# Performance work log

Hardware: AMD Instinct MI355X
Metric: run time of the kernel (lower is better)

## Reference

```python
import jax, jax.numpy as jnp
import numpy as np

B, N = 32, 64
ATTR, STATE, REL, GDIM = 4, 8, 4, 32
NF = 128

def _ln(x, w, b, eps=1e-5):
    mu = jnp.mean(x, axis=-1, keepdims=True)
    var = jnp.mean((x - mu) ** 2, axis=-1, keepdims=True)
    return (x - mu) * jax.lax.rsqrt(var + eps) * w + b

def setup_inputs() -> dict:
    key = jax.random.key(0)
    ks = iter(jax.random.split(key, 32))
    d = {}
    d['attrs'] = jax.random.normal(next(ks), (B, N, ATTR), jnp.float32)
    d['states'] = jax.random.normal(next(ks), (B, N, STATE), jnp.float32)
    d['actions'] = jnp.zeros((B, N, 4), jnp.float32)  # action=False, unused
    d['rel_attrs'] = jax.random.normal(next(ks), (B, N, N, REL), jnp.float32)
    def w(shape):
        return jax.random.normal(next(ks), shape, jnp.float32) * 0.05
    d['oe_w0'] = w((NF, ATTR + STATE)); d['oe_b0'] = jnp.zeros((NF,), jnp.float32)
    d['oe_w1'] = w((NF, NF));            d['oe_b1'] = jnp.zeros((NF,), jnp.float32)
    d['re_w0'] = w((NF, STATE + REL + 2 * ATTR)); d['re_b0'] = jnp.zeros((NF,), jnp.float32)
    d['re_w1'] = w((NF, NF));            d['re_b1'] = jnp.zeros((NF,), jnp.float32)
    d['rp_w'] = w((NF, NF + 2 * NF));    d['rp_b'] = jnp.zeros((NF,), jnp.float32)
    d['rp_lnw'] = jnp.ones((NF,), jnp.float32); d['rp_lnb'] = jnp.zeros((NF,), jnp.float32)
    d['pp_w'] = w((NF, 2 * NF));         d['pp_b'] = jnp.zeros((NF,), jnp.float32)
    d['pp_lnw'] = jnp.ones((NF,), jnp.float32); d['pp_lnb'] = jnp.zeros((NF,), jnp.float32)
    d['pr_w0'] = w((NF, NF));            d['pr_b0'] = jnp.zeros((NF,), jnp.float32)
    d['pr_w1'] = w((GDIM, NF));          d['pr_b1'] = jnp.zeros((GDIM,), jnp.float32)
    d['pstep'] = 2
    return d

def reference(attrs, states, actions, rel_attrs,
              oe_w0, oe_b0, oe_w1, oe_b1,
              re_w0, re_b0, re_w1, re_b1,
              rp_w, rp_b, rp_lnw, rp_lnb,
              pp_w, pp_b, pp_lnw, pp_lnb,
              pr_w0, pr_b0, pr_w1, pr_b1, pstep):
    lin = lambda x, w, b: jnp.einsum('...i,oi->...o', x, w) + b
    # ---- encode nodes: [B,N,attr+state] -> [B,N,NF] (action=False) ----
    obj_in = jnp.concatenate([attrs, states], axis=2)
    obj_encode = jax.nn.relu(lin(jax.nn.relu(lin(obj_in, oe_w0, oe_b0)), oe_w1, oe_b1))
    # ---- encode edges over dense N x N pairs ----
    rel_states = states[:, :, None, :] - states[:, None, :, :]        # B,N,N,state
    recv_attr = jnp.broadcast_to(attrs[:, :, None, :], (attrs.shape[0], attrs.shape[1], attrs.shape[1], attrs.shape[2]))
    send_attr = jnp.broadcast_to(attrs[:, None, :, :], recv_attr.shape)
    rel_in = jnp.concatenate([rel_attrs, rel_states, recv_attr, send_attr], axis=3)
    rel_encode = jax.nn.relu(lin(jax.nn.relu(lin(rel_in, re_w0, re_b0)), re_w1, re_b1))  # B,N,N,NF
    # ---- propagation steps ----
    for _ in range(pstep):
        sh = rel_encode.shape[:3] + (obj_encode.shape[-1],)
        recv = jnp.broadcast_to(obj_encode[:, :, None, :], sh)
        send = jnp.broadcast_to(obj_encode[:, None, :, :], sh)
        rel_effect = jax.nn.relu(_ln(lin(jnp.concatenate([rel_encode, recv, send], axis=3), rp_w, rp_b), rp_lnw, rp_lnb))
        rel_agg = rel_effect.sum(axis=2)                               # B,N,NF
        obj_encode = jax.nn.relu(_ln(lin(jnp.concatenate([obj_encode, rel_agg], axis=2), pp_w, pp_b), pp_lnw, pp_lnb))
    # ---- predict + tanh (state_encoder has tanh=True) ----
    out = lin(jax.nn.relu(lin(obj_encode, pr_w0, pr_b0)), pr_w1, pr_b1)
    return jnp.tanh(out)
```

## Files before the change

kernel.cpp:

```cpp
#include <hip/hip_runtime.h>
#include <hip/hip_bf16.h>


#define ROWS 2048
typedef unsigned short u16;
typedef unsigned int u32;
typedef __attribute__((ext_vector_type(8))) short bf16x8;
typedef __attribute__((ext_vector_type(4))) float f32x4;

__device__ __forceinline__ float bsu(u16 u) { return __uint_as_float(((u32)u) << 16); }
__device__ __forceinline__ u16 f2b(float f) {
    u32 u = __float_as_uint(f);
    u32 r = (u + 0x7fffu + ((u >> 16) & 1u)) >> 16;
    return (u16)r;
}
__device__ __forceinline__ u32 pk2(float a, float b) {
    __hip_bfloat162 h = __float22bfloat162_rn(float2{a, b});
    union { __hip_bfloat162 h; u32 u; } c; c.h = h; return c.u;
}
__device__ __forceinline__ bf16x8 ldcvt8(const float* __restrict__ p) {
    float4 a = *(const float4*)p;
    float4 b = *(const float4*)(p + 4);
    union { u32 u[4]; bf16x8 v; } x;
    x.u[0] = pk2(a.x, a.y); x.u[1] = pk2(a.z, a.w);
    x.u[2] = pk2(b.x, b.y); x.u[3] = pk2(b.z, b.w);
    return x.v;
}

__global__ __launch_bounds__(256)
void k_node(const float* __restrict__ attrs, const float* __restrict__ states,
            const float* __restrict__ oe_w0, const float* __restrict__ oe_b0,
            const float* __restrict__ oe_w1, const float* __restrict__ oe_b1,
            const float* __restrict__ re_w0, const float* __restrict__ re_b0,
            const float* __restrict__ rp_w,  const float* __restrict__ rp_b,
            const float* __restrict__ re_w1, const float* __restrict__ pp_w,
            const float* __restrict__ pr_w0, const float* __restrict__ pr_w1,
            u16* __restrict__ re_w1b, u16* __restrict__ web, u16* __restrict__ pp_wb,
            u16* __restrict__ wrecvb, u16* __restrict__ wsendb,
            u16* __restrict__ pr_w0b, u16* __restrict__ pr_w1b,
            u16* __restrict__ objb, float* __restrict__ nr, float* __restrict__ ns,
            float* __restrict__ recvT, float* __restrict__ sendT)
{
    const int r0 = blockIdx.x * 16;
    const int t = threadIdx.x;
    __shared__ float xs[16][12];
    __shared__ float w0s[1536];
    __shared__ float rw0s[2560];
    __shared__ __align__(16) u16 hb[16 * 136];
    __shared__ __align__(16) u16 ob[16 * 136];

    {
        int gid = blockIdx.x * 256 + t;
        for (int i = gid; i < 118784; i += 32768) {
            int idx = i;
            if (idx < 16384) { re_w1b[idx] = f2b(re_w1[idx]); continue; }
            idx -= 16384;
            if (idx < 16384) { web[idx] = f2b(rp_w[(idx >> 7) * 384 + (idx & 127)]); continue; }
            idx -= 16384;
            if (idx < 32768) { pp_wb[idx] = f2b(pp_w[idx]); continue; }
            idx -= 32768;
            if (idx < 16384) { wrecvb[idx] = f2b(rp_w[(idx >> 7) * 384 + 128 + (idx & 127)]); continue; }
            idx -= 16384;
            if (idx < 16384) { wsendb[idx] = f2b(rp_w[(idx >> 7) * 384 + 256 + (idx & 127)]); continue; }
            idx -= 16384;
            if (idx < 16384) { pr_w0b[idx] = f2b(pr_w0[idx]); continue; }
            idx -= 16384;
            pr_w1b[idx] = f2b(pr_w1[idx]);
        }
    }

    if (t < 192) { int row = t / 12, c = t - row * 12;
        xs[row][c] = (c < 4) ? attrs[(r0 + row) * 4 + c] : states[(r0 + row) * 8 + (c - 4)]; }
    for (int i = t; i < 1536; i += 256) w0s[i] = oe_w0[i];
    for (int i = t; i < 2560; i += 256) rw0s[i] = re_w0[i];
    __syncthreads();

    for (int e = t; e < 2048; e += 256) {
        int row = e >> 7, o = e & 127;
        float h = oe_b0[o];
#pragma unroll
        for (int k = 0; k < 12; k++) h += w0s[o * 12 + k] * xs[row][k];
        hb[row * 136 + o] = f2b(fmaxf(h, 0.f));
        float s0 = 0.f, a0 = 0.f, a1 = 0.f;
#pragma unroll
        for (int k = 0; k < 8; k++) s0 += rw0s[o * 20 + 4 + k] * xs[row][4 + k];
#pragma unroll
        for (int k = 0; k < 4; k++) {
            a0 += rw0s[o * 20 + 12 + k] * xs[row][k];
            a1 += rw0s[o * 20 + 16 + k] * xs[row][k];
        }
        nr[(r0 + row) * 128 + o] = s0 + a0 + re_b0[o];
        ns[(r0 + row) * 128 + o] = a1 - s0;
    }
    __syncthreads();

    const int wave = t >> 6, lane = t & 63, tx = lane & 15, quad = lane >> 4;

    bf16x8 afr[4];
#pragma unroll
    for (int kk = 0; kk < 4; kk++) afr[kk] = *(const bf16x8*)&hb[tx * 136 + kk * 32 + quad * 8];
    f32x4 acc[2]; acc[0] = (f32x4){0.f,0.f,0.f,0.f}; acc[1] = acc[0];
#pragma unroll
    for (int ot = 0; ot < 2; ot++) {
        int o = (wave * 2 + ot) * 16 + tx;
#pragma unroll
        for (int kk = 0; kk < 4; kk++) {
            bf16x8 bfr = ldcvt8(&oe_w1[o * 128 + kk * 32 + quad * 8]);
            acc[ot] = __builtin_amdgcn_mfma_f32_16x16x32_bf16(afr[kk], bfr, acc[ot], 0, 0, 0);
        }
    }
#pragma unroll
    for (int ot = 0; ot < 2; ot++) {
        int o = (wave * 2 + ot) * 16 + tx;
        float bia = oe_b1[o];
#pragma unroll
        for (int r = 0; r < 4; r++)
            ob[(quad * 4 + r) * 136 + o] = f2b(fmaxf(acc[ot][r] + bia, 0.f));
    }
    __syncthreads();
    { int m = t >> 4, c = t & 15;
      *(uint4*)&objb[(r0 + m) * 128 + c * 8] = *(const uint4*)&ob[m * 136 + c * 8]; }

#pragma unroll
    for (int kk = 0; kk < 4; kk++) afr[kk] = *(const bf16x8*)&ob[tx * 136 + kk * 32 + quad * 8];
    f32x4 ar[2], an[2];
    ar[0] = (f32x4){0.f,0.f,0.f,0.f}; ar[1] = ar[0]; an[0] = ar[0]; an[1] = ar[0];
#pragma unroll
    for (int ot = 0; ot < 2; ot++) {
        int o = (wave * 2 + ot) * 16 + tx;
#pragma unroll
        for (int kk = 0; kk < 4; kk++) {
            bf16x8 br = ldcvt8(&rp_w[o * 384 + 128 + kk * 32 + quad * 8]);
            ar[ot] = __builtin_amdgcn_mfma_f32_16x16x32_bf16(afr[kk], br, ar[ot], 0, 0, 0);
            bf16x8 bs = ldcvt8(&rp_w[o * 384 + 256 + kk * 32 + quad * 8]);
            an[ot] = __builtin_amdgcn_mfma_f32_16x16x32_bf16(afr[kk], bs, an[ot], 0, 0, 0);
        }
    }
#pragma unroll
    for (int ot = 0; ot < 2; ot++) {
        int o = (wave * 2 + ot) * 16 + tx;
        float rb = rp_b[o];
#pragma unroll
        for (int r = 0; r < 4; r++) {
            recvT[(r0 + quad * 4 + r) * 128 + o] = ar[ot][r] + rb;
            sendT[(r0 + quad * 4 + r) * 128 + o] = an[ot][r];
        }
    }
}

__global__ __launch_bounds__(256, 4)
void k_edge_fused(const float* __restrict__ rel_attrs,
                  const float* __restrict__ re_w0, const u16* __restrict__ re_w1b,
                  const u16* __restrict__ web, const float* __restrict__ re_b1,
                  const float* __restrict__ rp_lnw, const float* __restrict__ rp_lnb,
                  const float* __restrict__ nr, const float* __restrict__ ns,
                  const float* __restrict__ recvT, const float* __restrict__ sendT,
                  u16* __restrict__ Ebuf, u16* __restrict__ aggb)
{
    const int blkg = blockIdx.x;
    const int b = blkg >> 6;
    const int t = threadIdx.x;
    __shared__ __align__(16) u16 hsb[64 * 144];
    __shared__ float lnws[128], lnbs[128];
    __shared__ float redS[256], redQ[256];

    if (t < 128) { lnws[t] = rp_lnw[t]; lnbs[t] = rp_lnb[t]; }

    {
        const int o0 = (t & 15) * 8;
        const int jb = t >> 4;
        float4 nr0 = *(const float4*)&nr[blkg * 128 + o0];
        float4 nr1 = *(const float4*)&nr[blkg * 128 + o0 + 4];
        float4 wreg[8];
#pragma unroll
        for (int k = 0; k < 8; k++) wreg[k] = *(const float4*)&re_w0[(o0 + k) * 20];
#pragma unroll
        for (int it = 0; it < 4; it++) {
            int j = jb + it * 16;
            float4 ra = *(const float4*)&rel_attrs[((size_t)blkg * 64 + j) * 4];
            const float* nsp = &ns[(b * 64 + j) * 128 + o0];
            float4 na = *(const float4*)nsp;
            float4 nb = *(const float4*)(nsp + 4);
            float v[8];
            v[0] = nr0.x + na.x; v[1] = nr0.y + na.y; v[2] = nr0.z + na.z; v[3] = nr0.w + na.w;
            v[4] = nr1.x + nb.x; v[5] = nr1.y + nb.y; v[6] = nr1.z + nb.z; v[7] = nr1.w + nb.w;
#pragma unroll
            for (int k = 0; k < 8; k++) {
                v[k] += wreg[k].x * ra.x + wreg[k].y * ra.y + wreg[k].z * ra.z + wreg[k].w * ra.w;
                v[k] = fmaxf(v[k], 0.f);
            }
            union { u32 u[4]; uint4 q; } p;
            p.u[0] = pk2(v[0], v[1]); p.u[1] = pk2(v[2], v[3]);
            p.u[2] = pk2(v[4], v[5]); p.u[3] = pk2(v[6], v[7]);
            *(uint4*)&hsb[j * 144 + o0] = p.q;
        }
    }

    const int w = t >> 6, lane = t & 63, tx = lane & 15, quad = lane >> 4;
    const int ob = w * 32;

    bf16x8 b1[2][4];
#pragma unroll
    for (int ot = 0; ot < 2; ot++)
#pragma unroll
        for (int kk = 0; kk < 4; kk++)
            b1[ot][kk] = *(const bf16x8*)&re_w1b[(ob + ot * 16 + tx) * 128 + kk * 32 + quad * 8];
    __syncthreads();

    f32x4 acc[4][2];
#pragma unroll
    for (int jt = 0; jt < 4; jt++) { acc[jt][0] = (f32x4){0.f,0.f,0.f,0.f}; acc[jt][1] = acc[jt][0]; }
#pragma unroll
    for (int jt = 0; jt < 4; jt++) {
        bf16x8 afr[4];
#pragma unroll
        for (int kk = 0; kk < 4; kk++)
            afr[kk] = *(const bf16x8*)&hsb[(jt * 16 + tx) * 144 + kk * 32 + quad * 8];
#pragma unroll
        for (int ot = 0; ot < 2; ot++)
#pragma unroll
            for (int kk = 0; kk < 4; kk++)
                acc[jt][ot] = __builtin_amdgcn_mfma_f32_16x16x32_bf16(afr[kk], b1[ot][kk], acc[jt][ot], 0, 0, 0);
    }
    __syncthreads();

    {
        float bia0 = re_b1[ob + tx], bia1 = re_b1[ob + 16 + tx];
#pragma unroll
        for (int jt = 0; jt < 4; jt++)
#pragma unroll
            for (int r = 0; r < 4; r++) {
                int j = jt * 16 + quad * 4 + r;
                hsb[j * 144 + ob + tx]      = f2b(fmaxf(acc[jt][0][r] + bia0, 0.f));
                hsb[j * 144 + ob + 16 + tx] = f2b(fmaxf(acc[jt][1][r] + bia1, 0.f));
            }
    }
    bf16x8 b2[2][4];
#pragma unroll
    for (int ot = 0; ot < 2; ot++)
#pragma unroll
        for (int kk = 0; kk < 4; kk++)
            b2[ot][kk] = *(const bf16x8*)&web[(ob + ot * 16 + tx) * 128 + kk * 32 + quad * 8];
    __syncthreads();

    f32x4 acc2[4][2];
#pragma unroll
    for (int jt = 0; jt < 4; jt++) { acc2[jt][0] = (f32x4){0.f,0.f,0.f,0.f}; acc2[jt][1] = acc2[jt][0]; }
#pragma unroll
    for (int jt = 0; jt < 4; jt++) {
        bf16x8 afr[4];
#pragma unroll
        for (int kk = 0; kk < 4; kk++)
            afr[kk] = *(const bf16x8*)&hsb[(jt * 16 + tx) * 144 + kk * 32 + quad * 8];
#pragma unroll
        for (int ot = 0; ot < 2; ot++)
#pragma unroll
            for (int kk = 0; kk < 4; kk++)
                acc2[jt][ot] = __builtin_amdgcn_mfma_f32_16x16x32_bf16(afr[kk], b2[ot][kk], acc2[jt][ot], 0, 0, 0);
    }

#pragma unroll
    for (int jt = 0; jt < 4; jt++)
#pragma unroll
        for (int ot = 0; ot < 2; ot++) {
            uint2 ev;
            ev.x = pk2(acc2[jt][ot][0], acc2[jt][ot][1]);
            ev.y = pk2(acc2[jt][ot][2], acc2[jt][ot][3]);
            *(uint2*)(Ebuf + ((size_t)((blkg * 4 + jt) * 8 + (2 * w + ot)) * 64 + lane) * 4) = ev;
        }

    {
        float rv0 = recvT[blkg * 128 + ob + tx];
        float rv1 = recvT[blkg * 128 + ob + 16 + tx];
#pragma unroll
        for (int jt = 0; jt < 4; jt++)
#pragma unroll
            for (int r = 0; r < 4; r++) {
                int j = b * 64 + jt * 16 + quad * 4 + r;
                acc2[jt][0][r] += rv0 + sendT[j * 128 + ob + tx];
                acc2[jt][1][r] += rv1 + sendT[j * 128 + ob + 16 + tx];
            }
    }

#pragma unroll
    for (int jt = 0; jt < 4; jt++) {
        float s4[4], q4[4];
#pragma unroll
        for (int r = 0; r < 4; r++) {
            float a0 = acc2[jt][0][r], a1 = acc2[jt][1][r];
            s4[r] = a0 + a1; q4[r] = a0 * a0 + a1 * a1;
        }
#pragma unroll
        for (int m = 1; m < 16; m <<= 1)
#pragma unroll
            for (int r = 0; r < 4; r++) {
                s4[r] += __shfl_xor(s4[r], m, 64);
                q4[r] += __shfl_xor(q4[r], m, 64);
            }
        if (tx == 0)
#pragma unroll
            for (int r = 0; r < 4; r++) {
                redS[w * 64 + jt * 16 + quad * 4 + r] = s4[r];
                redQ[w * 64 + jt * 16 + quad * 4 + r] = q4[r];
            }
    }
    __syncthreads();

    {
        float lw0 = lnws[ob + tx], lb0 = lnbs[ob + tx];
        float lw1 = lnws[ob + 16 + tx], lb1 = lnbs[ob + 16 + tx];
        float ag0 = 0.f, ag1 = 0.f;
#pragma unroll
        for (int jt = 0; jt < 4; jt++)
#pragma unroll
            for (int r = 0; r < 4; r++) {
                int row = jt * 16 + quad * 4 + r;
                float ss = redS[row] + redS[64 + row] + redS[128 + row] + redS[192 + row];
                float qq = redQ[row] + redQ[64 + row] + redQ[128 + row] + redQ[192 + row];
                float mu = ss * (1.f / 128.f);
                float rsd = rsqrtf(qq * (1.f / 128.f) - mu * mu + 1e-5f);
                float z0 = (acc2[jt][0][r] - mu) * rsd * lw0 + lb0;
                float z1 = (acc2[jt][1][r] - mu) * rsd * lw1 + lb1;
                ag0 += fmaxf(z0, 0.f);
                ag1 += fmaxf(z1, 0.f);
            }
        ag0 += __shfl_xor(ag0, 16, 64); ag0 += __shfl_xor(ag0, 32, 64);
        ag1 += __shfl_xor(ag1, 16, 64); ag1 += __shfl_xor(ag1, 32, 64);
        if (quad == 0) {
            aggb[blkg * 128 + ob + tx]      = f2b(ag0);
            aggb[blkg * 128 + ob + 16 + tx] = f2b(ag1);
        }
    }
}

__global__ __launch_bounds__(256)
void k_prop_edge2(const u16* __restrict__ Ebuf,
                  const float* __restrict__ rp_lnw, const float* __restrict__ rp_lnb,
                  const float* __restrict__ recvT, const float* __restrict__ sendT,
                  u16* __restrict__ aggb)
{
    const int blk = blockIdx.x;
    const int b = blk >> 6;
    const int t = threadIdx.x;
    __shared__ float scr[16 * 132];
    __shared__ float lnws[128], lnbs[128];
    if (t < 128) { lnws[t] = rp_lnw[t]; lnbs[t] = rp_lnb[t]; }
    __syncthreads();

    const int wave = t >> 6, lane = t & 63, tx = lane & 15, quad = lane >> 4;
    const int tid = blk * 4 + wave;
    const int jrow = wave * 16 + quad * 4;

    float y[8][4];
#pragma unroll
    for (int oo = 0; oo < 8; oo++) {
        uint2 ev = *(const uint2*)(Ebuf + ((size_t)(tid * 8 + oo) * 64 + lane) * 4);
        const int o = oo * 16 + tx;
        float rv = recvT[blk * 128 + o];
        float e0 = bsu((u16)(ev.x & 0xffff)), e1 = bsu((u16)(ev.x >> 16));
        float e2 = bsu((u16)(ev.y & 0xffff)), e3 = bsu((u16)(ev.y >> 16));
        y[oo][0] = e0 + rv + sendT[(b * 64 + jrow + 0) * 128 + o];
        y[oo][1] = e1 + rv + sendT[(b * 64 + jrow + 1) * 128 + o];
        y[oo][2] = e2 + rv + sendT[(b * 64 + jrow + 2) * 128 + o];
        y[oo][3] = e3 + rv + sendT[(b * 64 + jrow + 3) * 128 + o];
    }
    float s[4], q[4];
#pragma unroll
    for (int r = 0; r < 4; r++) {
        s[r] = 0.f; q[r] = 0.f;
#pragma unroll
        for (int oo = 0; oo < 8; oo++) { s[r] += y[oo][r]; q[r] += y[oo][r] * y[oo][r]; }
    }
#pragma unroll
    for (int m = 1; m < 16; m <<= 1) {
#pragma unroll
        for (int r = 0; r < 4; r++) {
            s[r] += __shfl_xor(s[r], m, 64);
            q[r] += __shfl_xor(q[r], m, 64);
        }
    }
    float mu[4], rs[4];
#pragma unroll
    for (int r = 0; r < 4; r++) {
        mu[r] = s[r] * (1.f / 128.f);
        rs[r] = rsqrtf(q[r] * (1.f / 128.f) - mu[r] * mu[r] + 1e-5f);
    }
    float pa[8];
#pragma unroll
    for (int oo = 0; oo < 8; oo++) {
        const int o = oo * 16 + tx;
        float lw = lnws[o], lb = lnbs[o];
        float p = 0.f;
#pragma unroll
        for (int r = 0; r < 4; r++) {
            float z = (y[oo][r] - mu[r]) * rs[r] * lw + lb;
            p += fmaxf(z, 0.f);
        }
        pa[oo] = p;
    }
    const int grp = wave * 4 + quad;
#pragma unroll
    for (int oo = 0; oo < 8; oo++) scr[grp * 132 + oo * 16 + tx] = pa[oo];
    __syncthreads();
    if (t < 128) {
        float sum = 0.f;
#pragma unroll
        for (int gg = 0; gg < 16; gg++) sum += scr[gg * 132 + t];
        aggb[blk * 128 + t] = f2b(sum);
    }
}

__global__ __launch_bounds__(256)
void k_pn0(const u16* __restrict__ aggb,
           const u16* __restrict__ pp_wb, const float* __restrict__ pp_b,
           const float* __restrict__ pp_lnw, const float* __restrict__ pp_lnb,
           const u16* __restrict__ wrecvb, const u16* __restrict__ wsendb,
           const float* __restrict__ rp_b,
           u16* __restrict__ objb, float* __restrict__ recvT, float* __restrict__ sendT)
{
    const int r0 = blockIdx.x * 16;
    const int t = threadIdx.x;
    __shared__ __align__(16) u16 ab[16 * 264];
    __shared__ __align__(16) u16 ob[16 * 136];
    __shared__ float redS[64], redQ[64];

    for (int i = t; i < 512; i += 256) {
        int m = i >> 5, c = i & 31;
        uint4 v = (c < 16) ? *(const uint4*)&objb[(r0 + m) * 128 + (c & 15) * 8]
                           : *(const uint4*)&aggb[(r0 + m) * 128 + (c - 16) * 8];
        *(uint4*)&ab[m * 264 + c * 8] = v;
    }
    __syncthreads();

    const int wave = t >> 6, lane = t & 63, tx = lane & 15, quad = lane >> 4;
    bf16x8 afr[8];
#pragma unroll
    for (int kk = 0; kk < 8; kk++) afr[kk] = *(const bf16x8*)&ab[tx * 264 + kk * 32 + quad * 8];
    f32x4 acc[2]; acc[0] = (f32x4){0.f,0.f,0.f,0.f}; acc[1] = acc[0];
#pragma unroll
    for (int ot = 0; ot < 2; ot++) {
        int o = (wave * 2 + ot) * 16 + tx;
#pragma unroll
        for (int kk = 0; kk < 8; kk++) {
            bf16x8 bfr = *(const bf16x8*)&pp_wb[o * 256 + kk * 32 + quad * 8];
            acc[ot] = __builtin_amdgcn_mfma_f32_16x16x32_bf16(afr[kk], bfr, acc[ot], 0, 0, 0);
        }
    }
#pragma unroll
    for (int ot = 0; ot < 2; ot++) {
        float bia = pp_b[(wave * 2 + ot) * 16 + tx];
#pragma unroll
        for (int r = 0; r < 4; r++) acc[ot][r] += bia;
    }

    float s[4], q[4];
#pragma unroll
    for (int r = 0; r < 4; r++) {
        s[r] = acc[0][r] + acc[1][r];
        q[r] = acc[0][r] * acc[0][r] + acc[1][r] * acc[1][r];
    }
#pragma unroll
    for (int m = 1; m < 16; m <<= 1) {
#pragma unroll
        for (int r = 0; r < 4; r++) {
            s[r] += __shfl_xor(s[r], m, 64);
            q[r] += __shfl_xor(q[r], m, 64);
        }
    }
    if (tx == 0) {
#pragma unroll
        for (int r = 0; r < 4; r++) {
            redS[wave * 16 + quad * 4 + r] = s[r];
            redQ[wave * 16 + quad * 4 + r] = q[r];
        }
    }
    __syncthreads();
    float mu[4], rs[4];
#pragma unroll
    for (int r = 0; r < 4; r++) {
        int m = quad * 4 + r;
        float ss = redS[m] + redS[16 + m] + redS[32 + m] + redS[48 + m];
        float qq = redQ[m] + redQ[16 + m] + redQ[32 + m] + redQ[48 + m];
        mu[r] = ss * (1.f / 128.f);
        rs[r] = rsqrtf(qq * (1.f / 128.f) - mu[r] * mu[r] + 1e-5f);
    }
#pragma unroll
    for (int ot = 0; ot < 2; ot++) {
        int o = (wave * 2 + ot) * 16 + tx;
        float lw = pp_lnw[o], lb = pp_lnb[o];
#pragma unroll
        for (int r = 0; r < 4; r++) {
            float z = (acc[ot][r] - mu[r]) * rs[r] * lw + lb;
            ob[(quad * 4 + r) * 136 + o] = f2b(fmaxf(z, 0.f));
        }
    }
    __syncthreads();
    { int m = t >> 4, c = t & 15;
      *(uint4*)&objb[(r0 + m) * 128 + c * 8] = *(const uint4*)&ob[m * 136 + c * 8]; }

    bf16x8 af2[4];
#pragma unroll
    for (int kk = 0; kk < 4; kk++) af2[kk] = *(const bf16x8*)&ob[tx * 136 + kk * 32 + quad * 8];
    f32x4 ar[2], an[2];
    ar[0] = (f32x4){0.f,0.f,0.f,0.f}; ar[1] = ar[0]; an[0] = ar[0]; an[1] = ar[0];
#pragma unroll
    for (int ot = 0; ot < 2; ot++) {
        int o = (wave * 2 + ot) * 16 + tx;
#pragma unroll
        for (int kk = 0; kk < 4; kk++) {
            bf16x8 br = *(const bf16x8*)&wrecvb[o * 128 + kk * 32 + quad * 8];
            ar[ot] = __builtin_amdgcn_mfma_f32_16x16x32_bf16(af2[kk], br, ar[ot], 0, 0, 0);
            bf16x8 bs = *(const bf16x8*)&wsendb[o * 128 + kk * 32 + quad * 8];
            an[ot] = __builtin_amdgcn_mfma_f32_16x16x32_bf16(af2[kk], bs, an[ot], 0, 0, 0);
        }
    }
#pragma unroll
    for (int ot = 0; ot < 2; ot++) {
        int o = (wave * 2 + ot) * 16 + tx;
        float rb = rp_b[o];
#pragma unroll
        for (int r = 0; r < 4; r++) {
            recvT[(r0 + quad * 4 + r) * 128 + o] = ar[ot][r] + rb;
            sendT[(r0 + quad * 4 + r) * 128 + o] = an[ot][r];
        }
    }
}

__global__ __launch_bounds__(256)
void k_pn1pred(const u16* __restrict__ aggb,
               const u16* __restrict__ pp_wb, const float* __restrict__ pp_b,
               const float* __restrict__ pp_lnw, const float* __restrict__ pp_lnb,
               const u16* __restrict__ objb,
               const u16* __restrict__ pr_w0b, const float* __restrict__ pr_b0,
               const u16* __restrict__ pr_w1b, const float* __restrict__ pr_b1,
               float* __restrict__ out)
{
    const int r0 = blockIdx.x * 16;
    const int t = threadIdx.x;
    __shared__ __align__(16) u16 ab[16 * 264];
    __shared__ __align__(16) u16 ob[16 * 136];
    __shared__ __align__(16) u16 hb2[16 * 136];
    __shared__ float redS[64], redQ[64];

    for (int i = t; i < 512; i += 256) {
        int m = i >> 5, c = i & 31;
        uint4 v = (c < 16) ? *(const uint4*)&objb[(r0 + m) * 128 + (c & 15) * 8]
                           : *(const uint4*)&aggb[(r0 + m) * 128 + (c - 16) * 8];
        *(uint4*)&ab[m * 264 + c * 8] = v;
    }
    __syncthreads();

    const int wave = t >> 6, lane = t & 63, tx = lane & 15, quad = lane >> 4;
    bf16x8 afr[8];
#pragma unroll
    for (int kk = 0; kk < 8; kk++) afr[kk] = *(const bf16x8*)&ab[tx * 264 + kk * 32 + quad * 8];
    f32x4 acc[2]; acc[0] = (f32x4){0.f,0.f,0.f,0.f}; acc[1] = acc[0];
#pragma unroll
    for (int ot = 0; ot < 2; ot++) {
        int o = (wave * 2 + ot) * 16 + tx;
#pragma unroll
        for (int kk = 0; kk < 8; kk++) {
            bf16x8 bfr = *(const bf16x8*)&pp_wb[o * 256 + kk * 32 + quad * 8];
            acc[ot] = __builtin_amdgcn_mfma_f32_16x16x32_bf16(afr[kk], bfr, acc[ot], 0, 0, 0);
        }
    }
#pragma unroll
    for (int ot = 0; ot < 2; ot++) {
        float bia = pp_b[(wave * 2 + ot) * 16 + tx];
#pragma unroll
        for (int r = 0; r < 4; r++) acc[ot][r] += bia;
    }

    float s[4], q[4];
#pragma unroll
    for (int r = 0; r < 4; r++) {
        s[r] = acc[0][r] + acc[1][r];
        q[r] = acc[0][r] * acc[0][r] + acc[1][r] * acc[1][r];
    }
#pragma unroll
    for (int m = 1; m < 16; m <<= 1) {
#pragma unroll
        for (int r = 0; r < 4; r++) {
            s[r] += __shfl_xor(s[r], m, 64);
            q[r] += __shfl_xor(q[r], m, 64);
        }
    }
    if (tx == 0) {
#pragma unroll
        for (int r = 0; r < 4; r++) {
            redS[wave * 16 + quad * 4 + r] = s[r];
            redQ[wave * 16 + quad * 4 + r] = q[r];
        }
    }
    __syncthreads();
    float mu[4], rs[4];
#pragma unroll
    for (int r = 0; r < 4; r++) {
        int m = quad * 4 + r;
        float ss = redS[m] + redS[16 + m] + redS[32 + m] + redS[48 + m];
        float qq = redQ[m] + redQ[16 + m] + redQ[32 + m] + redQ[48 + m];
        mu[r] = ss * (1.f / 128.f);
        rs[r] = rsqrtf(qq * (1.f / 128.f) - mu[r] * mu[r] + 1e-5f);
    }
#pragma unroll
    for (int ot = 0; ot < 2; ot++) {
        int o = (wave * 2 + ot) * 16 + tx;
        float lw = pp_lnw[o], lb = pp_lnb[o];
#pragma unroll
        for (int r = 0; r < 4; r++) {
            float z = (acc[ot][r] - mu[r]) * rs[r] * lw + lb;
            ob[(quad * 4 + r) * 136 + o] = f2b(fmaxf(z, 0.f));
        }
    }
    __syncthreads();

    bf16x8 af2[4];
#pragma unroll
    for (int kk = 0; kk < 4; kk++) af2[kk] = *(const bf16x8*)&ob[tx * 136 + kk * 32 + quad * 8];
    f32x4 ah[2]; ah[0] = (f32x4){0.f,0.f,0.f,0.f}; ah[1] = ah[0];
#pragma unroll
    for (int ot = 0; ot < 2; ot++) {
        int o = (wave * 2 + ot) * 16 + tx;
#pragma unroll
        for (int kk = 0; kk < 4; kk++) {
            bf16x8 bfr = *(const bf16x8*)&pr_w0b[o * 128 + kk * 32 + quad * 8];
            ah[ot] = __builtin_amdgcn_mfma_f32_16x16x32_bf16(af2[kk], bfr, ah[ot], 0, 0, 0);
        }
    }
#pragma unroll
    for (int ot = 0; ot < 2; ot++) {
        int o = (wave * 2 + ot) * 16 + tx;
        float bia = pr_b0[o];
#pragma unroll
        for (int r = 0; r < 4; r++)
            hb2[(quad * 4 + r) * 136 + o] = f2b(fmaxf(ah[ot][r] + bia, 0.f));
    }
    __syncthreads();

    if (wave < 2) {
        bf16x8 af3[4];
#pragma unroll
        for (int kk = 0; kk < 4; kk++) af3[kk] = *(const bf16x8*)&hb2[tx * 136 + kk * 32 + quad * 8];
        f32x4 a2 = (f32x4){0.f,0.f,0.f,0.f};
        int o = wave * 16 + tx;
#pragma unroll
        for (int kk = 0; kk < 4; kk++) {
            bf16x8 bfr = *(const bf16x8*)&pr_w1b[o * 128 + kk * 32 + quad * 8];
            a2 = __builtin_amdgcn_mfma_f32_16x16x32_bf16(af3[kk], bfr, a2, 0, 0, 0);
        }
        float bia = pr_b1[o];
#pragma unroll
        for (int r = 0; r < 4; r++)
            out[(r0 + quad * 4 + r) * 32 + o] = tanhf(a2[r] + bia);
    }
}

extern "C" void kernel_launch(void* const* d_in, const int* in_sizes, int n_in,
                              void* d_out, int out_size, void* d_ws, size_t ws_size,
                              hipStream_t stream)
{
    const float* attrs    = (const float*)d_in[0];
    const float* states   = (const float*)d_in[1];
    const float* rel_attrs= (const float*)d_in[3];
    const float* oe_w0 = (const float*)d_in[4];
    const float* oe_b0 = (const float*)d_in[5];
    const float* oe_w1 = (const float*)d_in[6];
    const float* oe_b1 = (const float*)d_in[7];
    const float* re_w0 = (const float*)d_in[8];
    const float* re_b0 = (const float*)d_in[9];
    const float* re_w1 = (const float*)d_in[10];
    const float* re_b1 = (const float*)d_in[11];
    const float* rp_w  = (const float*)d_in[12];
    const float* rp_b  = (const float*)d_in[13];
    const float* rp_lnw= (const float*)d_in[14];
    const float* rp_lnb= (const float*)d_in[15];
    const float* pp_w  = (const float*)d_in[16];
    const float* pp_b  = (const float*)d_in[17];
    const float* pp_lnw= (const float*)d_in[18];
    const float* pp_lnb= (const float*)d_in[19];
    const float* pr_w0 = (const float*)d_in[20];
    const float* pr_b0 = (const float*)d_in[21];
    const float* pr_w1 = (const float*)d_in[22];
    const float* pr_b1 = (const float*)d_in[23];

    float* ws    = (float*)d_ws;
    float* nr    = ws;
    float* ns    = nr    + ROWS * 128;
    float* recvT = ns    + ROWS * 128;
    float* sendT = recvT + ROWS * 128;
    u16* re_w1b = (u16*)(sendT + ROWS * 128);
    u16* web    = re_w1b + 16384;
    u16* pp_wb  = web    + 16384;
    u16* wrecvb = pp_wb  + 32768;
    u16* wsendb = wrecvb + 16384;
    u16* pr_w0b = wsendb + 16384;
    u16* pr_w1b = pr_w0b + 16384;
    u16* objb   = pr_w1b + 4096;
    u16* aggb   = objb + ROWS * 128;
    u16* Ebuf   = aggb + ROWS * 128;

    k_node<<<128, 256, 0, stream>>>(attrs, states, oe_w0, oe_b0, oe_w1, oe_b1,
                                    re_w0, re_b0, rp_w, rp_b,
                                    re_w1, pp_w, pr_w0, pr_w1,
                                    re_w1b, web, pp_wb, wrecvb, wsendb, pr_w0b, pr_w1b,
                                    objb, nr, ns, recvT, sendT);
    k_edge_fused<<<2048, 256, 0, stream>>>(rel_attrs, re_w0, re_w1b, web, re_b1,
                                           rp_lnw, rp_lnb, nr, ns, recvT, sendT,
                                           Ebuf, aggb);
    k_pn0<<<128, 256, 0, stream>>>(aggb, pp_wb, pp_b, pp_lnw, pp_lnb,
                                   wrecvb, wsendb, rp_b, objb, recvT, sendT);
    k_prop_edge2<<<2048, 256, 0, stream>>>(Ebuf, rp_lnw, rp_lnb, recvT, sendT, aggb);
    k_pn1pred<<<128, 256, 0, stream>>>(aggb, pp_wb, pp_b, pp_lnw, pp_lnb, objb,
                                       pr_w0b, pr_b0, pr_w1b, pr_b1, (float*)d_out);
}
```

Before: 184.7 us.

## Split edge-fused kernel across two half-blocks per receiver with partial aggregation buffers

```diff
diff --git a/kernel.cpp b/kernel.cpp
--- a/kernel.cpp
+++ b/kernel.cpp
@@ -155,14 +155,16 @@
                   const float* __restrict__ rp_lnw, const float* __restrict__ rp_lnb,
                   const float* __restrict__ nr, const float* __restrict__ ns,
                   const float* __restrict__ recvT, const float* __restrict__ sendT,
-                  u16* __restrict__ Ebuf, u16* __restrict__ aggb)
+                  u16* __restrict__ Ebuf, float* __restrict__ aggpa, float* __restrict__ aggpb)
 {
-    const int blkg = blockIdx.x;
+    const int bid = blockIdx.x;
+    const int blkg = bid >> 1;
+    const int half = bid & 1;
     const int b = blkg >> 6;
     const int t = threadIdx.x;
-    __shared__ __align__(16) u16 hsb[64 * 144];
+    __shared__ __align__(16) u16 hsb[32 * 144];
     __shared__ float lnws[128], lnbs[128];
-    __shared__ float redS[256], redQ[256];
+    __shared__ float redS[128], redQ[128];
 
     if (t < 128) { lnws[t] = rp_lnw[t]; lnbs[t] = rp_lnb[t]; }
 
@@ -175,10 +177,11 @@
 #pragma unroll
         for (int k = 0; k < 8; k++) wreg[k] = *(const float4*)&re_w0[(o0 + k) * 20];
 #pragma unroll
-        for (int it = 0; it < 4; it++) {
+        for (int it = 0; it < 2; it++) {
             int j = jb + it * 16;
-            float4 ra = *(const float4*)&rel_attrs[((size_t)blkg * 64 + j) * 4];
-            const float* nsp = &ns[(b * 64 + j) * 128 + o0];
+            int jg = half * 32 + j;
+            float4 ra = *(const float4*)&rel_attrs[((size_t)blkg * 64 + jg) * 4];
+            const float* nsp = &ns[(b * 64 + jg) * 128 + o0];
             float4 na = *(const float4*)nsp;
             float4 nb = *(const float4*)(nsp + 4);
             float v[8];
@@ -207,11 +210,11 @@
             b1[ot][kk] = *(const bf16x8*)&re_w1b[(ob + ot * 16 + tx) * 128 + kk * 32 + quad * 8];
     __syncthreads();
 
-    f32x4 acc[4][2];
-#pragma unroll
-    for (int jt = 0; jt < 4; jt++) { acc[jt][0] = (f32x4){0.f,0.f,0.f,0.f}; acc[jt][1] = acc[jt][0]; }
-#pragma unroll
-    for (int jt = 0; jt < 4; jt++) {
+    f32x4 acc[2][2];
+#pragma unroll
+    for (int jt = 0; jt < 2; jt++) { acc[jt][0] = (f32x4){0.f,0.f,0.f,0.f}; acc[jt][1] = acc[jt][0]; }
+#pragma unroll
+    for (int jt = 0; jt < 2; jt++) {
         bf16x8 afr[4];
 #pragma unroll
         for (int kk = 0; kk < 4; kk++)
@@ -227,7 +230,7 @@
     {
         float bia0 = re_b1[ob + tx], bia1 = re_b1[ob + 16 + tx];
 #pragma unroll
-        for (int jt = 0; jt < 4; jt++)
+        for (int jt = 0; jt < 2; jt++)
 #pragma unroll
             for (int r = 0; r < 4; r++) {
                 int j = jt * 16 + quad * 4 + r;
@@ -243,11 +246,11 @@
             b2[ot][kk] = *(const bf16x8*)&web[(ob + ot * 16 + tx) * 128 + kk * 32 + quad * 8];
     __syncthreads();
 
-    f32x4 acc2[4][2];
-#pragma unroll
-    for (int jt = 0; jt < 4; jt++) { acc2[jt][0] = (f32x4){0.f,0.f,0.f,0.f}; acc2[jt][1] = acc2[jt][0]; }
-#pragma unroll
-    for (int jt = 0; jt < 4; jt++) {
+    f32x4 acc2[2][2];
+#pragma unroll
+    for (int jt = 0; jt < 2; jt++) { acc2[jt][0] = (f32x4){0.f,0.f,0.f,0.f}; acc2[jt][1] = acc2[jt][0]; }
+#pragma unroll
+    for (int jt = 0; jt < 2; jt++) {
         bf16x8 afr[4];
 #pragma unroll
         for (int kk = 0; kk < 4; kk++)
@@ -260,30 +263,30 @@
     }
 
 #pragma unroll
-    for (int jt = 0; jt < 4; jt++)
+    for (int jt = 0; jt < 2; jt++)
 #pragma unroll
         for (int ot = 0; ot < 2; ot++) {
             uint2 ev;
             ev.x = pk2(acc2[jt][ot][0], acc2[jt][ot][1]);
             ev.y = pk2(acc2[jt][ot][2], acc2[jt][ot][3]);
-            *(uint2*)(Ebuf + ((size_t)((blkg * 4 + jt) * 8 + (2 * w + ot)) * 64 + lane) * 4) = ev;
+            *(uint2*)(Ebuf + ((size_t)((blkg * 4 + half * 2 + jt) * 8 + (2 * w + ot)) * 64 + lane) * 4) = ev;
         }
 
     {
         float rv0 = recvT[blkg * 128 + ob + tx];
         float rv1 = recvT[blkg * 128 + ob + 16 + tx];
 #pragma unroll
-        for (int jt = 0; jt < 4; jt++)
+        for (int jt = 0; jt < 2; jt++)
 #pragma unroll
             for (int r = 0; r < 4; r++) {
-                int j = b * 64 + jt * 16 + quad * 4 + r;
+                int j = b * 64 + half * 32 + jt * 16 + quad * 4 + r;
                 acc2[jt][0][r] += rv0 + sendT[j * 128 + ob + tx];
                 acc2[jt][1][r] += rv1 + sendT[j * 128 + ob + 16 + tx];
             }
     }
 
 #pragma unroll
-    for (int jt = 0; jt < 4; jt++) {
+    for (int jt = 0; jt < 2; jt++) {
         float s4[4], q4[4];
 #pragma unroll
         for (int r = 0; r < 4; r++) {
@@ -300,8 +303,8 @@
         if (tx == 0)
 #pragma unroll
             for (int r = 0; r < 4; r++) {
-                redS[w * 64 + jt * 16 + quad * 4 + r] = s4[r];
-                redQ[w * 64 + jt * 16 + quad * 4 + r] = q4[r];
+                redS[w * 32 + jt * 16 + quad * 4 + r] = s4[r];
+                redQ[w * 32 + jt * 16 + quad * 4 + r] = q4[r];
             }
     }
     __syncthreads();
@@ -311,12 +314,12 @@
         float lw1 = lnws[ob + 16 + tx], lb1 = lnbs[ob + 16 + tx];
         float ag0 = 0.f, ag1 = 0.f;
 #pragma unroll
-        for (int jt = 0; jt < 4; jt++)
+        for (int jt = 0; jt < 2; jt++)
 #pragma unroll
             for (int r = 0; r < 4; r++) {
                 int row = jt * 16 + quad * 4 + r;
-                float ss = redS[row] + redS[64 + row] + redS[128 + row] + redS[192 + row];
-                float qq = redQ[row] + redQ[64 + row] + redQ[128 + row] + redQ[192 + row];
+                float ss = redS[row] + redS[32 + row] + redS[64 + row] + redS[96 + row];
+                float qq = redQ[row] + redQ[32 + row] + redQ[64 + row] + redQ[96 + row];
                 float mu = ss * (1.f / 128.f);
                 float rsd = rsqrtf(qq * (1.f / 128.f) - mu * mu + 1e-5f);
                 float z0 = (acc2[jt][0][r] - mu) * rsd * lw0 + lb0;
@@ -327,8 +330,9 @@
         ag0 += __shfl_xor(ag0, 16, 64); ag0 += __shfl_xor(ag0, 32, 64);
         ag1 += __shfl_xor(ag1, 16, 64); ag1 += __shfl_xor(ag1, 32, 64);
         if (quad == 0) {
-            aggb[blkg * 128 + ob + tx]      = f2b(ag0);
-            aggb[blkg * 128 + ob + 16 + tx] = f2b(ag1);
+            float* aggp = half ? aggpb : aggpa;
+            aggp[blkg * 128 + ob + tx]      = ag0;
+            aggp[blkg * 128 + ob + 16 + tx] = ag1;
         }
     }
 }
@@ -411,7 +415,7 @@
 }
 
 __global__ __launch_bounds__(256)
-void k_pn0(const u16* __restrict__ aggb,
+void k_pn0(const float* __restrict__ aggpa, const float* __restrict__ aggpb,
            const u16* __restrict__ pp_wb, const float* __restrict__ pp_b,
            const float* __restrict__ pp_lnw, const float* __restrict__ pp_lnb,
            const u16* __restrict__ wrecvb, const u16* __restrict__ wsendb,
@@ -426,9 +430,23 @@
 
     for (int i = t; i < 512; i += 256) {
         int m = i >> 5, c = i & 31;
-        uint4 v = (c < 16) ? *(const uint4*)&objb[(r0 + m) * 128 + (c & 15) * 8]
-                           : *(const uint4*)&aggb[(r0 + m) * 128 + (c - 16) * 8];
-        *(uint4*)&ab[m * 264 + c * 8] = v;
+        if (c < 16) {
+            *(uint4*)&ab[m * 264 + c * 8] = *(const uint4*)&objb[(r0 + m) * 128 + (c & 15) * 8];
+        } else {
+            int cc = c - 16;
+            const float* pa = &aggpa[(r0 + m) * 128 + cc * 8];
+            const float* pb = &aggpb[(r0 + m) * 128 + cc * 8];
+            float4 a0 = *(const float4*)pa;
+            float4 a1 = *(const float4*)(pa + 4);
+            float4 b0 = *(const float4*)pb;
+            float4 b1 = *(const float4*)(pb + 4);
+            union { u32 u[4]; uint4 q; } p;
+            p.u[0] = pk2(a0.x + b0.x, a0.y + b0.y);
+            p.u[1] = pk2(a0.z + b0.z, a0.w + b0.w);
+            p.u[2] = pk2(a1.x + b1.x, a1.y + b1.y);
+            p.u[3] = pk2(a1.z + b1.z, a1.w + b1.w);
+            *(uint4*)&ab[m * 264 + c * 8] = p.q;
+        }
     }
     __syncthreads();
 
@@ -636,7 +654,6 @@
             hb2[(quad * 4 + r) * 136 + o] = f2b(fmaxf(ah[ot][r] + bia, 0.f));
     }
     __syncthreads();
-
     if (wave < 2) {
         bf16x8 af3[4];
 #pragma unroll
@@ -688,7 +705,9 @@
     float* ns    = nr    + ROWS * 128;
     float* recvT = ns    + ROWS * 128;
     float* sendT = recvT + ROWS * 128;
-    u16* re_w1b = (u16*)(sendT + ROWS * 128);
+    float* aggpa = sendT + ROWS * 128;
+    float* aggpb = aggpa + ROWS * 128;
+    u16* re_w1b = (u16*)(aggpb + ROWS * 128);
     u16* web    = re_w1b + 16384;
     u16* pp_wb  = web    + 16384;
     u16* wrecvb = pp_wb  + 32768;
@@ -704,10 +723,10 @@
                                     re_w1, pp_w, pr_w0, pr_w1,
                                     re_w1b, web, pp_wb, wrecvb, wsendb, pr_w0b, pr_w1b,
                                     objb, nr, ns, recvT, sendT);
-    k_edge_fused<<<2048, 256, 0, stream>>>(rel_attrs, re_w0, re_w1b, web, re_b1,
+    k_edge_fused<<<4096, 256, 0, stream>>>(rel_attrs, re_w0, re_w1b, web, re_b1,
                                            rp_lnw, rp_lnb, nr, ns, recvT, sendT,
-                                           Ebuf, aggb);
-    k_pn0<<<128, 256, 0, stream>>>(aggb, pp_wb, pp_b, pp_lnw, pp_lnb,
+                                           Ebuf, aggpa, aggpb);
+    k_pn0<<<128, 256, 0, stream>>>(aggpa, aggpb, pp_wb, pp_b, pp_lnw, pp_lnb,
                                    wrecvb, wsendb, rp_b, objb, recvT, sendT);
     k_prop_edge2<<<2048, 256, 0, stream>>>(Ebuf, rp_lnw, rp_lnb, recvT, sendT, aggb);
     k_pn1pred<<<128, 256, 0, stream>>>(aggb, pp_wb, pp_b, pp_lnw, pp_lnb, objb,
```

Result: slower. 199.5 us (+8.0%).
